# Kernel optimization log

Measured on AMD Instinct MI355X. Metric: run time of the kernel, lower is better.

The kernel has to match this reference:

```python
import jax, jax.numpy as jnp
import numpy as np

N = 50000
E = 800000
IN_F = 128
HID_F = 128
OUT_F = 128
BN_EPS = 1e-5


def make_quaternion_mul(kernel):
    # kernel: [d_in//4, d_out]; returns hamilton: [d_in, d_out]
    r, i, j, k = jnp.split(kernel, 4, axis=1)
    r2 = jnp.concatenate([r, -i, -j, -k], axis=0)
    i2 = jnp.concatenate([i, r, -k, j], axis=0)
    j2 = jnp.concatenate([j, k, r, -i], axis=0)
    k2 = jnp.concatenate([k, -j, i, r], axis=0)
    return jnp.concatenate([r2, i2, j2, k2], axis=1)


def setup_inputs() -> dict:
    key = jax.random.key(0)
    k1, k2, k3, k4, k5, k6 = jax.random.split(key, 6)
    stdv = np.sqrt(6.0 / (IN_F // 4 + HID_F)).astype(np.float32)
    inputs = {
        "input": jax.random.normal(k1, (N, IN_F), dtype=jnp.float32),
        "adj_row": jnp.sort(jax.random.randint(k2, (E,), 0, N, dtype=jnp.int32)),
        "adj_col": jax.random.randint(k3, (E,), 0, N, dtype=jnp.int32),
        "adj_val": jax.random.uniform(k4, (E,), dtype=jnp.float32),
        "weight1": jax.random.uniform(k5, (IN_F // 4, HID_F), minval=-stdv, maxval=stdv, dtype=jnp.float32),
        "weight2": jax.random.uniform(k6, (HID_F // 4, OUT_F), minval=-stdv, maxval=stdv, dtype=jnp.float32),
        "gamma": jnp.ones((OUT_F,), dtype=jnp.float32),
        "beta": jnp.zeros((OUT_F,), dtype=jnp.float32),
    }
    return inputs


def reference(input, adj_row, adj_col, adj_val, weight1, weight2, gamma, beta):
    hamilton1 = make_quaternion_mul(weight1)  # [IN_F, HID_F]
    hamilton2 = make_quaternion_mul(weight2)  # [HID_F, OUT_F]
    out1 = jnp.tanh(input @ hamilton1)        # [N, HID_F]
    out2 = out1 @ hamilton2                   # [N, OUT_F]
    # sparse adj (COO) x dense: out[i] = sum_e val[e] * out2[col[e]] for row[e]==i
    gathered = adj_val[:, None] * out2[adj_col]  # [E, OUT_F]
    agg = jax.ops.segment_sum(gathered, adj_row, num_segments=N)  # [N, OUT_F]
    # BatchNorm1d (training mode): per-feature stats over nodes, biased var
    mean = jnp.mean(agg, axis=0)
    var = jnp.var(agg, axis=0)
    return gamma * (agg - mean) * jax.lax.rsqrt(var + BN_EPS) + beta
```

## Files before the change

### kernel.cpp

```cpp
#include <hip/hip_runtime.h>
#include <cstddef>
#include <cstdint>

#define F 128
#define LDK 136
#define AGG_BLOCKS 1280
#define MID_BLOCKS 64

typedef __attribute__((ext_vector_type(8))) short short8;
typedef __attribute__((ext_vector_type(4))) float f32x4;

__device__ __forceinline__ short f2bf(float f) {
  uint32_t u = __float_as_uint(f);
  uint32_t r = u + 0x7FFFu + ((u >> 16) & 1u);
  return (short)(r >> 16);
}
__device__ __forceinline__ float bf2f(short h) {
  return __uint_as_float(((uint32_t)(uint16_t)h) << 16);
}

__global__ __launch_bounds__(256) void setup_kernel(
    const float* __restrict__ w1, const float* __restrict__ w2,
    short* __restrict__ Hpk, const int* __restrict__ adj_row,
    const int* __restrict__ adj_col, const float* __restrict__ adj_val,
    int* __restrict__ rowptr, uint2* __restrict__ cv, int E, int N) {
  if (blockIdx.x < 16) {
    int idx = blockIdx.x * 256 + threadIdx.x;
    int m = idx >> 11;
    int kt = (idx >> 9) & 3;
    int ct = (idx >> 6) & 7;
    int l = idx & 63;
    int col = ct * 16 + (l & 15);
    const float* w = m ? w2 : w1;
    short hi[8], lo[8];
#pragma unroll
    for (int j = 0; j < 8; ++j) {
      int row = kt * 32 + (l >> 4) * 8 + j;
      int rb = row >> 5, cb = col >> 5;
      int neg = (0x284E >> (cb * 4 + rb)) & 1;
      float v = w[(row & 31) * 128 + (rb ^ cb) * 32 + (col & 31)];
      v = neg ? -v : v;
      short h = f2bf(v);
      hi[j] = h;
      lo[j] = f2bf(v - bf2f(h));
    }
    size_t b0 = ((((size_t)m * 2 + 0) * 4 + kt) * 8 + ct) * 64 + l;
    size_t b1 = ((((size_t)m * 2 + 1) * 4 + kt) * 8 + ct) * 64 + l;
    *(short8*)&Hpk[b0 * 8] = *(short8*)hi;
    *(short8*)&Hpk[b1 * 8] = *(short8*)lo;
  } else {
    int e = (blockIdx.x - 16) * 256 + threadIdx.x;
    if (e >= E) return;
    cv[e] = make_uint2((uint32_t)adj_col[e], __float_as_uint(adj_val[e]));
    int r = adj_row[e];
    int rprev = (e == 0) ? -1 : adj_row[e - 1];
    for (int q = rprev + 1; q <= r; ++q) rowptr[q] = e;
    if (e == E - 1) {
      for (int q = r + 1; q <= N; ++q) rowptr[q] = E;
    }
  }
}

__global__ __launch_bounds__(256) void gemm_mfma(
    const float* __restrict__ input, const short* __restrict__ Hpk,
    short* __restrict__ out2b, int N) {
  __shared__ short lds[4][16 * LDK];
  const int t = threadIdx.x;
  const int w = t >> 6, l = t & 63;
  const int lr = l & 15, lg = l >> 4;
  const int grow0 = blockIdx.x * 64 + w * 16;
  short* hid = &lds[w][0];

  short8 a1h[4];
  {
    int arow = grow0 + lr;
    if (arow >= N) arow = N - 1;
    const float* xr = &input[(size_t)arow * F];
#pragma unroll
    for (int kt = 0; kt < 4; ++kt) {
      float xv[8];
      *(float4*)&xv[0] = *(const float4*)&xr[kt * 32 + lg * 8];
      *(float4*)&xv[4] = *(const float4*)&xr[kt * 32 + lg * 8 + 4];
#pragma unroll
      for (int j = 0; j < 8; ++j) ((short*)&a1h[kt])[j] = f2bf(xv[j]);
    }
  }

  f32x4 acc[8];
#pragma unroll
  for (int ct = 0; ct < 8; ++ct) acc[ct] = (f32x4){0.f, 0.f, 0.f, 0.f};
#pragma unroll
  for (int kt = 0; kt < 4; ++kt) {
#pragma unroll
    for (int ct = 0; ct < 8; ++ct) {
      short8 bh = *(const short8*)&Hpk[((((size_t)0 * 4 + kt) * 8 + ct) * 64 + l) * 8];
      short8 bl = *(const short8*)&Hpk[((((size_t)1 * 4 + kt) * 8 + ct) * 64 + l) * 8];
      acc[ct] = __builtin_amdgcn_mfma_f32_16x16x32_bf16(a1h[kt], bl, acc[ct], 0, 0, 0);
      acc[ct] = __builtin_amdgcn_mfma_f32_16x16x32_bf16(a1h[kt], bh, acc[ct], 0, 0, 0);
    }
  }

#pragma unroll
  for (int ct = 0; ct < 8; ++ct)
#pragma unroll
    for (int r = 0; r < 4; ++r)
      hid[(lg * 4 + r) * LDK + ct * 16 + lr] = f2bf(tanhf(acc[ct][r]));

  short8 a2h[4];
#pragma unroll
  for (int kt = 0; kt < 4; ++kt)
    a2h[kt] = *(short8*)&hid[lr * LDK + kt * 32 + lg * 8];

#pragma unroll
  for (int ct = 0; ct < 8; ++ct) acc[ct] = (f32x4){0.f, 0.f, 0.f, 0.f};
#pragma unroll
  for (int kt = 0; kt < 4; ++kt) {
#pragma unroll
    for (int ct = 0; ct < 8; ++ct) {
      short8 bh = *(const short8*)&Hpk[((((size_t)2 * 4 + kt) * 8 + ct) * 64 + l) * 8];
      short8 bl = *(const short8*)&Hpk[((((size_t)3 * 4 + kt) * 8 + ct) * 64 + l) * 8];
      acc[ct] = __builtin_amdgcn_mfma_f32_16x16x32_bf16(a2h[kt], bl, acc[ct], 0, 0, 0);
      acc[ct] = __builtin_amdgcn_mfma_f32_16x16x32_bf16(a2h[kt], bh, acc[ct], 0, 0, 0);
    }
  }

#pragma unroll
  for (int ct = 0; ct < 8; ++ct)
#pragma unroll
    for (int r = 0; r < 4; ++r)
      hid[(lg * 4 + r) * LDK + ct * 16 + lr] = f2bf(acc[ct][r]);
#pragma unroll
  for (int i = 0; i < 4; ++i) {
    int chunk = i * 64 + l;
    int row = chunk >> 4, pos = chunk & 15;
    int grow = grow0 + row;
    if (grow < N)
      *(short8*)&out2b[(size_t)grow * F + pos * 8] = *(short8*)&hid[row * LDK + pos * 8];
  }
}

__global__ __launch_bounds__(256) void agg_rows6(
    const uint32_t* __restrict__ out2u,
    const int* __restrict__ rowptr, const uint2* __restrict__ cv,
    float* __restrict__ agg, float* __restrict__ partials, int N) {
  const int t = threadIdx.x;
  const int w = t >> 6, lane = t & 63;
  const int sub = lane >> 4;
  const int fl4 = (lane & 15) * 4;
  const int wid = blockIdx.x * 4 + w;
  const int nw = gridDim.x * 4;
  float ssum[8], ssq[8];
#pragma unroll
  for (int j = 0; j < 8; ++j) { ssum[j] = 0.f; ssq[j] = 0.f; }

  for (int pr = wid; pr * 2 < N; pr += nw) {
    const int rowA = pr * 2;
    const bool hasB = rowA + 1 < N;
    const int sA = rowptr[rowA];
    const int eAe = rowptr[rowA + 1];
    const int eBe = hasB ? rowptr[rowA + 2] : eAe;
    const int sB = eAe;

    float accA[8], accB[8];
#pragma unroll
    for (int j = 0; j < 8; ++j) { accA[j] = 0.f; accB[j] = 0.f; }

    int eA = sA, eB = sB;
    while (eA < eAe || eB < eBe) {
      float vA[4], vB[4];
      uint32_t cA[4], cB[4];
#pragma unroll
      for (int q = 0; q < 4; ++q) {
        int ee = eA + q * 4 + sub;
        bool val = ee < eAe;
        int idx = val ? ee : (eAe - 1);
        idx = idx < 0 ? 0 : idx;
        uint2 p = cv[idx];
        cA[q] = p.x;
        vA[q] = val ? __uint_as_float(p.y) : 0.f;
      }
#pragma unroll
      for (int q = 0; q < 4; ++q) {
        int ee = eB + q * 4 + sub;
        bool val = ee < eBe;
        int idx = val ? ee : (eBe - 1);
        idx = idx < 0 ? 0 : idx;
        uint2 p = cv[idx];
        cB[q] = p.x;
        vB[q] = val ? __uint_as_float(p.y) : 0.f;
      }
      uint4 uA[4], uB[4];
#pragma unroll
      for (int q = 0; q < 4; ++q)
        uA[q] = *(const uint4*)&out2u[(size_t)(cA[q] * 64u + fl4)];
#pragma unroll
      for (int q = 0; q < 4; ++q)
        uB[q] = *(const uint4*)&out2u[(size_t)(cB[q] * 64u + fl4)];
#pragma unroll
      for (int q = 0; q < 4; ++q) {
#pragma unroll
        for (int k = 0; k < 4; ++k) {
          uint32_t ua = ((const uint32_t*)&uA[q])[k];
          uint32_t ub = ((const uint32_t*)&uB[q])[k];
          accA[2 * k]     = fmaf(vA[q], __uint_as_float(ua << 16), accA[2 * k]);
          accA[2 * k + 1] = fmaf(vA[q], __uint_as_float(ua & 0xFFFF0000u), accA[2 * k + 1]);
          accB[2 * k]     = fmaf(vB[q], __uint_as_float(ub << 16), accB[2 * k]);
          accB[2 * k + 1] = fmaf(vB[q], __uint_as_float(ub & 0xFFFF0000u), accB[2 * k + 1]);
        }
      }
      eA += 16;
      eB += 16;
    }
#pragma unroll
    for (int j = 0; j < 8; ++j) {
      accA[j] += __shfl_xor(accA[j], 16, 64);
      accA[j] += __shfl_xor(accA[j], 32, 64);
      accB[j] += __shfl_xor(accB[j], 16, 64);
      accB[j] += __shfl_xor(accB[j], 32, 64);
    }
    if (sub == 0) {
      *(float4*)&agg[(size_t)rowA * F + fl4 * 2] = make_float4(accA[0], accA[1], accA[2], accA[3]);
      *(float4*)&agg[(size_t)rowA * F + fl4 * 2 + 4] = make_float4(accA[4], accA[5], accA[6], accA[7]);
#pragma unroll
      for (int j = 0; j < 8; ++j) {
        ssum[j] += accA[j];
        ssq[j] = fmaf(accA[j], accA[j], ssq[j]);
      }
      if (hasB) {
        *(float4*)&agg[(size_t)(rowA + 1) * F + fl4 * 2] = make_float4(accB[0], accB[1], accB[2], accB[3]);
        *(float4*)&agg[(size_t)(rowA + 1) * F + fl4 * 2 + 4] = make_float4(accB[4], accB[5], accB[6], accB[7]);
#pragma unroll
        for (int j = 0; j < 8; ++j) {
          ssum[j] += accB[j];
          ssq[j] = fmaf(accB[j], accB[j], ssq[j]);
        }
      }
    }
  }

  __shared__ float ls[4][128];
  __shared__ float lq[4][128];
  if (sub == 0) {
#pragma unroll
    for (int j = 0; j < 8; ++j) {
      ls[w][fl4 * 2 + j] = ssum[j];
      lq[w][fl4 * 2 + j] = ssq[j];
    }
  }
  __syncthreads();
  if (t < 128) {
    float S = ls[0][t] + ls[1][t] + ls[2][t] + ls[3][t];
    float Q = lq[0][t] + lq[1][t] + lq[2][t] + lq[3][t];
    float* dst = &partials[(size_t)blockIdx.x * 256];
    dst[t] = S;
    dst[128 + t] = Q;
  }
}

__global__ __launch_bounds__(256) void mid_reduce(
    const float* __restrict__ partials, float* __restrict__ mid, int nb) {
  const int k = blockIdx.x, t = threadIdx.x;
  const int per = nb / MID_BLOCKS;
  float s = 0.f;
#pragma unroll 4
  for (int i = 0; i < per; ++i)
    s += partials[(size_t)(k * per + i) * 256 + t];
  mid[(size_t)k * 256 + t] = s;
}

__global__ __launch_bounds__(256) void finalize_stats3(
    const float* __restrict__ mid, const float* __restrict__ gamma,
    const float* __restrict__ beta, float* __restrict__ ss, float invN) {
  const int t = threadIdx.x;
  float s = 0.f;
#pragma unroll 8
  for (int b = 0; b < MID_BLOCKS; ++b) s += mid[(size_t)b * 256 + t];
  __shared__ float tot[256];
  tot[t] = s;
  __syncthreads();
  if (t < 128) {
    float mean = tot[t] * invN;
    float var = tot[128 + t] * invN - mean * mean;
    float inv = rsqrtf(var + 1e-5f);
    float sc = gamma[t] * inv;
    ss[t] = sc;
    ss[128 + t] = beta[t] - mean * sc;
  }
}

__global__ __launch_bounds__(256) void bn_apply(
    float* __restrict__ out, const float* __restrict__ ss, int total4) {
  int idx = blockIdx.x * 256 + threadIdx.x;
  if (idx >= total4) return;
  int f4 = (idx & 31) * 4;
  float4 v = *(float4*)&out[(size_t)idx * 4];
  float4 sc = *(const float4*)&ss[f4];
  float4 sh = *(const float4*)&ss[128 + f4];
  v.x = fmaf(v.x, sc.x, sh.x);
  v.y = fmaf(v.y, sc.y, sh.y);
  v.z = fmaf(v.z, sc.z, sh.z);
  v.w = fmaf(v.w, sc.w, sh.w);
  *(float4*)&out[(size_t)idx * 4] = v;
}

extern "C" void kernel_launch(void* const* d_in, const int* in_sizes, int n_in,
                              void* d_out, int out_size, void* d_ws, size_t ws_size,
                              hipStream_t stream) {
  (void)n_in; (void)out_size; (void)ws_size;
  const float* input  = (const float*)d_in[0];
  const int*  adj_row = (const int*)d_in[1];
  const int*  adj_col = (const int*)d_in[2];
  const float* adj_val = (const float*)d_in[3];
  const float* w1 = (const float*)d_in[4];
  const float* w2 = (const float*)d_in[5];
  const float* gamma = (const float*)d_in[6];
  const float* beta  = (const float*)d_in[7];
  const int N = in_sizes[0] / F;
  const int E = in_sizes[1];

  char* ws = (char*)d_ws;
  short* Hpk = (short*)(ws);
  float* ss = (float*)(ws + 131072);
  float* partials = (float*)(ws + 132096);
  float* mid = (float*)(ws + 2229248);
  int* rowptr = (int*)(ws + 2294784);
  uint2* cv = (uint2*)(ws + 2499584);
  size_t cv_bytes = ((size_t)E * 8 + 511) & ~(size_t)511;
  short* out2b = (short*)(ws + 2499584 + cv_bytes);
  float* agg = (float*)d_out;

  setup_kernel<<<16 + (E + 255) / 256, 256, 0, stream>>>(
      w1, w2, Hpk, adj_row, adj_col, adj_val, rowptr, cv, E, N);
  gemm_mfma<<<(N + 63) / 64, 256, 0, stream>>>(input, Hpk, out2b, N);
  agg_rows6<<<AGG_BLOCKS, 256, 0, stream>>>(
      (const uint32_t*)out2b, rowptr, cv, agg, partials, N);
  mid_reduce<<<MID_BLOCKS, 256, 0, stream>>>(partials, mid, AGG_BLOCKS);
  finalize_stats3<<<1, 256, 0, stream>>>(mid, gamma, beta, ss, 1.0f / (float)N);
  bn_apply<<<(N * 32 + 255) / 256, 256, 0, stream>>>(agg, ss, N * 32);
}
```

Measured before the change: 87.21 us.

## Stage Hamilton weights in LDS, widen GEMM blocks, prefetch rowptr in aggregation

The GEMM kernel now runs 512-thread blocks covering 128 rows and copies the packed bf16 Hamilton weights for each layer into 64 KB of shared memory, so each wave no longer re-reads them from global memory. The aggregation kernel loads the next row pair's rowptr bounds one iteration ahead to hide that load latency, and its grid grows from 1280 to 2048 blocks. The shared-memory staging adds barriers and a large LDS footprint that limits GEMM occupancy. The bigger aggregation grid also gives the downstream partial-sum reduction more partials to process.

```diff
diff --git a/kernel.cpp b/kernel.cpp
--- a/kernel.cpp
+++ b/kernel.cpp
@@ -4,7 +4,7 @@
 
 #define F 128
 #define LDK 136
-#define AGG_BLOCKS 1280
+#define AGG_BLOCKS 2048
 #define MID_BLOCKS 64
 
 typedef __attribute__((ext_vector_type(8))) short short8;
@@ -61,15 +61,22 @@
   }
 }
 
-__global__ __launch_bounds__(256) void gemm_mfma(
+__global__ __launch_bounds__(512) void gemm_mfma(
     const float* __restrict__ input, const short* __restrict__ Hpk,
     short* __restrict__ out2b, int N) {
-  __shared__ short lds[4][16 * LDK];
+  __shared__ short Hs[32768];
+  __shared__ short lds[8][16 * LDK];
   const int t = threadIdx.x;
   const int w = t >> 6, l = t & 63;
   const int lr = l & 15, lg = l >> 4;
-  const int grow0 = blockIdx.x * 64 + w * 16;
+  const int grow0 = blockIdx.x * 128 + w * 16;
   short* hid = &lds[w][0];
+
+#pragma unroll
+  for (int i = 0; i < 8; ++i) {
+    int idx = i * 512 + t;
+    *(short8*)&Hs[idx * 8] = *(const short8*)&Hpk[idx * 8];
+  }
 
   short8 a1h[4];
   {
@@ -85,6 +92,7 @@
       for (int j = 0; j < 8; ++j) ((short*)&a1h[kt])[j] = f2bf(xv[j]);
     }
   }
+  __syncthreads();
 
   f32x4 acc[8];
 #pragma unroll
@@ -93,8 +101,8 @@
   for (int kt = 0; kt < 4; ++kt) {
 #pragma unroll
     for (int ct = 0; ct < 8; ++ct) {
-      short8 bh = *(const short8*)&Hpk[((((size_t)0 * 4 + kt) * 8 + ct) * 64 + l) * 8];
-      short8 bl = *(const short8*)&Hpk[((((size_t)1 * 4 + kt) * 8 + ct) * 64 + l) * 8];
+      short8 bh = *(const short8*)&Hs[(((0 * 4 + kt) * 8 + ct) * 64 + l) * 8];
+      short8 bl = *(const short8*)&Hs[(((1 * 4 + kt) * 8 + ct) * 64 + l) * 8];
       acc[ct] = __builtin_amdgcn_mfma_f32_16x16x32_bf16(a1h[kt], bl, acc[ct], 0, 0, 0);
       acc[ct] = __builtin_amdgcn_mfma_f32_16x16x32_bf16(a1h[kt], bh, acc[ct], 0, 0, 0);
     }
@@ -111,14 +119,22 @@
   for (int kt = 0; kt < 4; ++kt)
     a2h[kt] = *(short8*)&hid[lr * LDK + kt * 32 + lg * 8];
 
+  __syncthreads();
+#pragma unroll
+  for (int i = 0; i < 8; ++i) {
+    int idx = i * 512 + t;
+    *(short8*)&Hs[idx * 8] = *(const short8*)&Hpk[32768 + idx * 8];
+  }
+  __syncthreads();
+
 #pragma unroll
   for (int ct = 0; ct < 8; ++ct) acc[ct] = (f32x4){0.f, 0.f, 0.f, 0.f};
 #pragma unroll
   for (int kt = 0; kt < 4; ++kt) {
 #pragma unroll
     for (int ct = 0; ct < 8; ++ct) {
-      short8 bh = *(const short8*)&Hpk[((((size_t)2 * 4 + kt) * 8 + ct) * 64 + l) * 8];
-      short8 bl = *(const short8*)&Hpk[((((size_t)3 * 4 + kt) * 8 + ct) * 64 + l) * 8];
+      short8 bh = *(const short8*)&Hs[(((0 * 4 + kt) * 8 + ct) * 64 + l) * 8];
+      short8 bl = *(const short8*)&Hs[(((1 * 4 + kt) * 8 + ct) * 64 + l) * 8];
       acc[ct] = __builtin_amdgcn_mfma_f32_16x16x32_bf16(a2h[kt], bl, acc[ct], 0, 0, 0);
       acc[ct] = __builtin_amdgcn_mfma_f32_16x16x32_bf16(a2h[kt], bh, acc[ct], 0, 0, 0);
     }
@@ -139,7 +155,7 @@
   }
 }
 
-__global__ __launch_bounds__(256) void agg_rows6(
+__global__ __launch_bounds__(256) void agg_rows7(
     const uint32_t* __restrict__ out2u,
     const int* __restrict__ rowptr, const uint2* __restrict__ cv,
     float* __restrict__ agg, float* __restrict__ partials, int N) {
@@ -153,12 +169,25 @@
 #pragma unroll
   for (int j = 0; j < 8; ++j) { ssum[j] = 0.f; ssq[j] = 0.f; }
 
-  for (int pr = wid; pr * 2 < N; pr += nw) {
+  int pr = wid;
+  bool active = pr * 2 < N;
+  int sA = 0, eAe = 0, eBe = 0;
+  if (active) {
+    sA = rowptr[pr * 2];
+    eAe = rowptr[pr * 2 + 1];
+    eBe = (pr * 2 + 1 < N) ? rowptr[pr * 2 + 2] : eAe;
+  }
+  while (active) {
+    const int prn = pr + nw;
+    const bool actn = prn * 2 < N;
+    int sAn = 0, eAen = 0, eBen = 0;
+    if (actn) {
+      sAn = rowptr[prn * 2];
+      eAen = rowptr[prn * 2 + 1];
+      eBen = (prn * 2 + 1 < N) ? rowptr[prn * 2 + 2] : eAen;
+    }
     const int rowA = pr * 2;
     const bool hasB = rowA + 1 < N;
-    const int sA = rowptr[rowA];
-    const int eAe = rowptr[rowA + 1];
-    const int eBe = hasB ? rowptr[rowA + 2] : eAe;
     const int sB = eAe;
 
     float accA[8], accB[8];
@@ -236,6 +265,9 @@
         }
       }
     }
+    pr = prn;
+    sA = sAn; eAe = eAen; eBe = eBen;
+    active = actn;
   }
 
   __shared__ float ls[4][128];
@@ -331,8 +363,8 @@
 
   setup_kernel<<<16 + (E + 255) / 256, 256, 0, stream>>>(
       w1, w2, Hpk, adj_row, adj_col, adj_val, rowptr, cv, E, N);
-  gemm_mfma<<<(N + 63) / 64, 256, 0, stream>>>(input, Hpk, out2b, N);
-  agg_rows6<<<AGG_BLOCKS, 256, 0, stream>>>(
+  gemm_mfma<<<(N + 127) / 128, 512, 0, stream>>>(input, Hpk, out2b, N);
+  agg_rows7<<<AGG_BLOCKS, 256, 0, stream>>>(
       (const uint32_t*)out2b, rowptr, cv, agg, partials, N);
   mid_reduce<<<MID_BLOCKS, 256, 0, stream>>>(partials, mid, AGG_BLOCKS);
   finalize_stats3<<<1, 256, 0, stream>>>(mid, gamma, beta, ss, 1.0f / (float)N);
```

After: 83.64 us. 4.1% less time.
